# Optimization experiments

Measured on AMD Instinct MI355X. Metric: run time of the kernel, lower is better.

## Reference

```python
import jax, jax.numpy as jnp
import numpy as np

B, S, Dm, H, W, G = 2, 4096, 768, 12, 256, 16
HD = Dm // H
NEG = -10000.0


def _band_qk(q, k, w):
    # q,k: [B,S,H,D] -> banded scores [B,S,H,2w+1]; slot j = key position i-w+j
    Bq, Sq, Hq, Dq = q.shape
    nb = Sq // w
    qb = q.reshape(Bq, nb, w, Hq, Dq)
    kp = jnp.pad(k, ((0, 0), (w, w), (0, 0), (0, 0)))
    idx = (jnp.arange(nb) * w)[:, None] + jnp.arange(3 * w)[None, :]
    kb = kp[:, idx]                                    # [B,nb,3w,H,D]
    s = jnp.einsum('btxhd,btyhd->bthxy', qb, kb)       # [B,nb,H,w,3w]
    r = jnp.arange(w)[:, None]
    c = r + jnp.arange(2 * w + 1)[None, :]
    band = s[..., r, c]                                # [B,nb,H,w,2w+1]
    return band.transpose(0, 1, 3, 2, 4).reshape(Bq, Sq, Hq, 2 * w + 1)


def _band_pv(p, v, w):
    # p: [B,S,H,2w+1], v: [B,S,H,D] -> [B,S,H,D]
    Bp, Sp, Hp, _ = p.shape
    Dv = v.shape[-1]
    nb = Sp // w
    vp = jnp.pad(v, ((0, 0), (w, w), (0, 0), (0, 0)))
    idx = (jnp.arange(nb) * w)[:, None] + jnp.arange(3 * w)[None, :]
    vb = vp[:, idx]                                    # [B,nb,3w,H,D]
    pb = p.reshape(Bp, nb, w, Hp, 2 * w + 1).transpose(0, 1, 3, 2, 4)
    r = jnp.arange(w)[:, None]
    c = r + jnp.arange(2 * w + 1)[None, :]
    pband = jnp.zeros((Bp, nb, Hp, w, 3 * w), p.dtype).at[..., r, c].set(pb)
    out = jnp.einsum('bthxy,btyhd->btxhd', pband, vb)  # [B,nb,w,H,D]
    return out.reshape(Bp, Sp, Hp, Dv)


def setup_inputs() -> dict:
    key = jax.random.key(0)
    ks = jax.random.split(key, 13)
    inp = {'hidden_states': jax.random.normal(ks[0], (B, S, Dm), dtype=jnp.float32)}
    names = ['Wq', 'bq', 'Wk', 'bk', 'Wv', 'bv', 'Wqg', 'bqg', 'Wkg', 'bkg', 'Wvg', 'bvg']
    for i, n in enumerate(names):
        sh = (Dm, Dm) if n.startswith('W') else (Dm,)
        inp[n] = 0.02 * jax.random.normal(ks[i + 1], sh, dtype=jnp.float32)
    inp['n_global'] = G
    return inp


def reference(hidden_states, Wq, bq, Wk, bk, Wv, bv, Wqg, bqg, Wkg, bkg, Wvg, bvg, n_global):
    Bh, Sh, D = hidden_states.shape
    hd = D // H
    w, g = W, n_global
    scale = 1.0 / jnp.sqrt(jnp.float32(hd))
    q = ((hidden_states @ Wq + bq) * scale).reshape(Bh, Sh, H, hd)
    k = (hidden_states @ Wk + bk).reshape(Bh, Sh, H, hd)
    v = (hidden_states @ Wv + bv).reshape(Bh, Sh, H, hd)
    # banded local attention scores (mask_invalid_locations -> -inf outside seq)
    band = _band_qk(q, k, w)                           # [B,S,H,2w+1]
    i = jnp.arange(Sh)[:, None]
    j = jnp.arange(2 * w + 1)[None, :]
    kpos = i - w + j                                   # key position per window slot
    valid = (kpos >= 0) & (kpos < Sh)
    band = jnp.where(valid[None, :, None, :], band, -jnp.inf)
    # remove global keys from windowed attention (-10000 float mask)
    band = band + jnp.where(valid & (kpos < g), NEG, 0.0)[None, :, None, :]
    # global columns: every query attends to global keys (local k projection)
    sel = jnp.einsum('bihd,bghd->bihg', q, k[:, :g])
    logits = jnp.concatenate([sel, band], axis=-1)     # [B,S,H,g+2w+1]
    probs = jax.nn.softmax(logits.astype(jnp.float32), axis=-1)
    attn = jnp.einsum('bihg,bghd->bihd', probs[..., :g], v[:, :g])
    attn = attn + _band_pv(probs[..., g:], v, w)       # [B,S,H,hd]
    # global token rows: full attention with global projections
    qg = ((hidden_states[:, :g] @ Wqg + bqg) * scale).reshape(Bh, g, H, hd)
    kg = (hidden_states @ Wkg + bkg).reshape(Bh, Sh, H, hd)
    vg = (hidden_states @ Wvg + bvg).reshape(Bh, Sh, H, hd)
    gl = jnp.einsum('bghd,bshd->bhgs', qg, kg)
    gp = jax.nn.softmax(gl.astype(jnp.float32), axis=-1)
    out_g = jnp.einsum('bhgs,bshd->bghd', gp, vg)      # [B,g,H,hd]
    attn = attn.at[:, :g].set(out_g)
    return attn.reshape(Bh, Sh, D)
```

## Files before the change

kernel.cpp:

```cpp
#include <hip/hip_runtime.h>

constexpr int Bc = 2, Sc = 4096, Dmc = 768, Hc = 12, HDc = 64, Wc = 256, Gc = 16;
constexpr int NCHG = 64;
constexpr float LOG2E = 1.4426950408889634f;
constexpr float SCALE2q = 0.125f * LOG2E;
constexpr float NEG2c = -10000.0f * LOG2E;

typedef __attribute__((ext_vector_type(8))) short s16x8;
typedef __attribute__((ext_vector_type(4))) short s16x4;
typedef __attribute__((ext_vector_type(4))) float f32x4;
typedef __attribute__((ext_vector_type(2))) unsigned int u32x2;

#define DEVINL __device__ __forceinline__

DEVINL float b2f(short x) {
  unsigned int u = ((unsigned int)(unsigned short)x) << 16;
  return __builtin_bit_cast(float, u);
}
DEVINL short f2b(float f) {
  unsigned int u = __builtin_bit_cast(unsigned int, f);
  unsigned int r = (u + 0x7fffu + ((u >> 16) & 1u)) >> 16;
  return (short)r;
}
DEVINL void gload16(const short* g, const short* l) {
  __builtin_amdgcn_global_load_lds(
      (const __attribute__((address_space(1))) void*)g,
      (__attribute__((address_space(3))) void*)l, 16, 0, 0);
}
DEVINL float max3f(float a, float b, float c) { return fmaxf(fmaxf(a, b), c); }

__global__ __launch_bounds__(256) void conv_bf16(
    const float* __restrict__ src, short* __restrict__ dst)
{
  const size_t i = ((size_t)blockIdx.x * 256 + threadIdx.x) * 8;
  f32x4 a = *(const f32x4*)(src + i);
  f32x4 c = *(const f32x4*)(src + i + 4);
  s16x8 r;
#pragma unroll
  for (int u = 0; u < 4; ++u) { r[u] = f2b(a[u]); r[4 + u] = f2b(c[u]); }
  *(s16x8*)(dst + i) = r;
}

__global__ __launch_bounds__(256) void transpose_w(
    const float* __restrict__ W0, const float* __restrict__ W1, const float* __restrict__ W2,
    short* __restrict__ T0, short* __restrict__ T1, short* __restrict__ T2)
{
  const float* W = blockIdx.z == 0 ? W0 : (blockIdx.z == 1 ? W1 : W2);
  short* T = blockIdx.z == 0 ? T0 : (blockIdx.z == 1 ? T1 : T2);
  __shared__ short t[32][33];
  const int k0 = blockIdx.x * 32, n0 = blockIdx.y * 32;
  const int a = threadIdx.x >> 3, cg = (threadIdx.x & 7) * 4;
  f32x4 v = *(const f32x4*)&W[(size_t)(k0 + a) * Dmc + n0 + cg];
#pragma unroll
  for (int u = 0; u < 4; ++u) t[a][cg + u] = f2b(v[u]);
  __syncthreads();
  s16x4 s;
#pragma unroll
  for (int u = 0; u < 4; ++u) s[u] = t[cg + u][a];
  *(s16x4*)&T[(size_t)(n0 + a) * Dmc + k0 + cg] = s;
}

__global__ __launch_bounds__(256) void gemm_fused(
    const short* __restrict__ X, const short* __restrict__ Wt,
    const float* __restrict__ b0, const float* __restrict__ b1, const float* __restrict__ b2,
    short* __restrict__ Y0, float scale0)
{
  __shared__ short lds[16384];
  char* ldsb = (char*)lds;
  const int tid = threadIdx.x, lane = tid & 63, wid = tid >> 6;
  const int gy = gridDim.y;

  const int rawd = blockIdx.x + 64 * blockIdx.y;
  const int wgid = (rawd & 7) * (gy * 8) + (rawd >> 3);
  const int mi0 = wgid / gy, ny = wgid - mi0 * gy;
  const int m0 = mi0 * 128;
  const int nch = ny / 6, ncol = (ny % 6) * 128;
  const int n0g = ny * 128;

  short* Y = Y0 + (size_t)nch * 6291456;
  const float* bias = nch == 0 ? b0 : (nch == 1 ? b1 : b2);
  const float scale = nch == 0 ? scale0 : 1.0f;

  const int lr = lane & 15, lq = lane >> 4;
  const int wm = (wid & 1) * 64, wn = (wid >> 1) * 64;

  const int l8 = lane >> 3, l7 = lane & 7;
  const int colsh = ((l7 * 16) ^ (l8 << 4)) >> 1;
  const short* Aptr[4];
  const short* Bptr[4];
#pragma unroll
  for (int i = 0; i < 4; ++i) {
    Aptr[i] = X  + (size_t)(m0  + wid * 32 + i * 8 + l8) * Dmc + colsh;
    Bptr[i] = Wt + (size_t)(n0g + wid * 32 + i * 8 + l8) * Dmc + colsh;
  }

  int arb[4][2], brb[4][2];
#pragma unroll
  for (int mi = 0; mi < 4; ++mi)
#pragma unroll
    for (int ks = 0; ks < 2; ++ks) {
      int row = wm + mi * 16 + lr;
      arb[mi][ks] = row * 128 + ((lq * 16 + ks * 64) ^ ((row & 7) << 4));
    }
#pragma unroll
  for (int ni = 0; ni < 4; ++ni)
#pragma unroll
    for (int ks = 0; ks < 2; ++ks) {
      int row = wn + ni * 16 + lr;
      brb[ni][ks] = 16384 + row * 128 + ((lq * 16 + ks * 64) ^ ((row & 7) << 4));
    }

  f32x4 acc[4][4] = {};

  for (int kt = 0; kt < 12; ++kt) {
    const int ko = kt * 64;
    if (kt) __syncthreads();
#pragma unroll
    for (int i = 0; i < 4; ++i) {
      gload16(Aptr[i] + ko, &lds[wid * 2048 + i * 512]);
      gload16(Bptr[i] + ko, &lds[8192 + wid * 2048 + i * 512]);
    }
    asm volatile("s_waitcnt vmcnt(0)" ::: "memory");
    __syncthreads();
#pragma unroll
    for (int ks = 0; ks < 2; ++ks) {
      s16x8 af[4], bf[4];
#pragma unroll
      for (int mi = 0; mi < 4; ++mi) af[mi] = *(const s16x8*)(ldsb + arb[mi][ks]);
#pragma unroll
      for (int ni = 0; ni < 4; ++ni) bf[ni] = *(const s16x8*)(ldsb + brb[ni][ks]);
#pragma unroll
      for (int mi = 0; mi < 4; ++mi)
#pragma unroll
        for (int ni = 0; ni < 4; ++ni)
          acc[mi][ni] = __builtin_amdgcn_mfma_f32_16x16x32_bf16(af[mi], bf[ni], acc[mi][ni], 0, 0, 0);
    }
  }

#pragma unroll
  for (int mi = 0; mi < 4; ++mi)
#pragma unroll
    for (int ni = 0; ni < 4; ++ni) {
      int col = ncol + wn + ni * 16 + lr;
      float bv_ = bias[col];
#pragma unroll
      for (int r = 0; r < 4; ++r) {
        int row = m0 + wm + mi * 16 + lq * 4 + r;
        Y[(size_t)row * Dmc + col] = f2b((acc[mi][ni][r] + bv_) * scale);
      }
    }
}

__global__ __launch_bounds__(256) void qg_proj(
    const float* __restrict__ hs, const float* __restrict__ Wqg,
    const float* __restrict__ bqg, short* __restrict__ qg)
{
  const int row = blockIdx.x;
  const int b = row / Gc, i = row % Gc;
  const int tid = threadIdx.x;
  const int n = blockIdx.y * 128 + (tid & 127);
  const int half = tid >> 7;
  __shared__ float x[Dmc];
  __shared__ float part[128];
  for (int c = tid; c < Dmc; c += 256)
    x[c] = b2f(f2b(hs[((size_t)(b * Sc + i)) * Dmc + c]));
  __syncthreads();
  float acc = 0.f;
#pragma unroll 4
  for (int c = half * 384; c < half * 384 + 384; ++c)
    acc = fmaf(x[c], b2f(f2b(Wqg[(size_t)c * Dmc + n])), acc);
  if (half) part[tid & 127] = acc;
  __syncthreads();
  if (!half)
    qg[(size_t)row * Dmc + n] = f2b((acc + part[tid] + bqg[n]) * SCALE2q);
}

__global__ __launch_bounds__(256) void local_attn_mfma(
    const short* __restrict__ q, const short* __restrict__ k,
    const short* __restrict__ v, float* __restrict__ out)
{
  const int raw = blockIdx.x + 64 * (blockIdx.y + 12 * blockIdx.z);
  const int swz = (raw & 7) * 192 + (raw >> 3);
  const int q0 = (swz & 63) * 64;
  const int h = (swz >> 6) % 12, b = swz / 768;
  const int tid = threadIdx.x, lane = tid & 63, wid = tid >> 6;

  __shared__ short Ks[4096];
  __shared__ short Vt[4096];
  __shared__ short Ps[4][1024];
  char* KsB = (char*)Ks;
  char* VtB = (char*)Vt;

  const int ql = lane & 15;
  const int lg = lane >> 4;
  const int qr = wid * 16 + ql;

  s16x8 qf[2];
  {
    const short* qp = q + ((size_t)(b * Sc + q0 + qr)) * Dmc + h * HDc + lg * 8;
    qf[0] = *(const s16x8*)qp;
    qf[1] = *(const s16x8*)(qp + 32);
  }

  f32x4 oacc[4] = {};
  float m_run = -INFINITY, l_run = 0.f;

  const int krow = tid >> 3, kcol16 = (tid & 7) * 16;
  const int vp = tid & 31, vo = tid >> 5;
  const size_t hoff = (size_t)h * HDc;
  const size_t brow = (size_t)b * Sc;

  const bool interior = (q0 >= 256) && (q0 <= Sc - 384);

  auto keyof = [&](int c) {
    int key = (c < Gc) ? c : q0 - 272 + c;
    return min(max(key, 0), Sc - 1);
  };

  const short *kp0, *kp1, *vp0, *vp1;
  s16x8 kreg0, kreg1, vreg0, vreg1;
  auto loadRegs = [&](int ch) {
    if (!interior || ch <= 1) {
      kp0 = k + (brow + keyof(ch * 64 + krow))       * Dmc + hoff + (kcol16 >> 1);
      kp1 = k + (brow + keyof(ch * 64 + 32 + krow))  * Dmc + hoff + (kcol16 >> 1);
      vp0 = v + (brow + keyof(ch * 64 + 2 * vp))      * Dmc + hoff + vo * 8;
      vp1 = v + (brow + keyof(ch * 64 + 2 * vp + 1))  * Dmc + hoff + vo * 8;
    } else {
      kp0 += 64 * Dmc; kp1 += 64 * Dmc; vp0 += 64 * Dmc; vp1 += 64 * Dmc;
    }
    kreg0 = *(const s16x8*)kp0;
    kreg1 = *(const s16x8*)kp1;
    vreg0 = *(const s16x8*)vp0;
    vreg1 = *(const s16x8*)vp1;
  };

  loadRegs(0);

  for (int ch = 0; ch < 10; ++ch) {
    __syncthreads();
    *(s16x8*)(KsB + krow * 128        + (kcol16 ^ ((krow & 7) << 4))) = kreg0;
    *(s16x8*)(KsB + (krow + 32) * 128 + (kcol16 ^ ((krow & 7) << 4))) = kreg1;
#pragma unroll
    for (int j = 0; j < 8; ++j) {
      int d = vo * 8 + j;
      unsigned int wrd = (unsigned int)(unsigned short)vreg0[j] |
                         ((unsigned int)(unsigned short)vreg1[j] << 16);
      *(unsigned int*)(VtB + d * 128 + ((4 * vp) ^ (j << 4))) = wrd;
    }
    if (ch < 9) loadRegs(ch + 1);
    __syncthreads();

    if (ch == 9 && wid != 3) continue;

    f32x4 sac[4] = {};
    __builtin_amdgcn_s_setprio(1);
#pragma unroll
    for (int kt = 0; kt < 4; ++kt) {
      int row = kt * 16 + ql;
#pragma unroll
      for (int sl = 0; sl < 2; ++sl) {
        s16x8 af = *(const s16x8*)(KsB + row * 128 + ((lg * 16 + sl * 64) ^ ((row & 7) << 4)));
        sac[kt] = __builtin_amdgcn_mfma_f32_16x16x32_bf16(af, qf[sl], sac[kt], 0, 0, 0);
      }
    }
    __builtin_amdgcn_s_setprio(0);

    bool needMask = (ch < 2) | (ch > 7) | (q0 < 272) | (q0 > Sc - 384);
    if (needMask) {
#pragma unroll
      for (int kt = 0; kt < 4; ++kt)
#pragma unroll
        for (int r = 0; r < 4; ++r) {
          int c = ch * 64 + kt * 16 + lg * 4 + r;
          if (c >= Gc) {
            float sv = sac[kt][r];
            int jj = c - Gc - qr;
            int kp2 = q0 - 272 + c;
            bool ok = (jj >= 0) & (jj <= 2 * Wc) & (kp2 >= 0) & (kp2 < Sc);
            sac[kt][r] = ok ? (sv + ((kp2 < Gc) ? NEG2c : 0.f)) : -INFINITY;
          }
        }
    }

    float t0 = max3f(sac[0][0], sac[0][1], sac[0][2]);
    float t1 = max3f(sac[0][3], sac[1][0], sac[1][1]);
    float t2 = max3f(sac[1][2], sac[1][3], sac[2][0]);
    float t3 = max3f(sac[2][1], sac[2][2], sac[2][3]);
    float t4 = max3f(sac[3][0], sac[3][1], sac[3][2]);
    float cm = fmaxf(max3f(t0, t1, t2), max3f(t3, t4, sac[3][3]));
    cm = fmaxf(cm, __shfl_xor(cm, 16));
    cm = fmaxf(cm, __shfl_xor(cm, 32));

    if (__all(cm <= m_run + 11.5f)) {
      float cl0 = 0.f, cl1 = 0.f, cl2 = 0.f, cl3 = 0.f;
#pragma unroll
      for (int kt = 0; kt < 4; ++kt) {
        float p0 = __builtin_amdgcn_exp2f(sac[kt][0] - m_run);
        float p1 = __builtin_amdgcn_exp2f(sac[kt][1] - m_run);
        float p2 = __builtin_amdgcn_exp2f(sac[kt][2] - m_run);
        float p3 = __builtin_amdgcn_exp2f(sac[kt][3] - m_run);
        sac[kt][0] = p0; sac[kt][1] = p1; sac[kt][2] = p2; sac[kt][3] = p3;
        cl0 += p0; cl1 += p1; cl2 += p2; cl3 += p3;
      }
      float cl = (cl0 + cl1) + (cl2 + cl3);
      cl += __shfl_xor(cl, 16);
      cl += __shfl_xor(cl, 32);
      l_run += cl;
    } else {
      float m_new = fmaxf(m_run, cm);
      float scale = __builtin_amdgcn_exp2f(m_run - m_new);
      float cl0 = 0.f, cl1 = 0.f, cl2 = 0.f, cl3 = 0.f;
#pragma unroll
      for (int kt = 0; kt < 4; ++kt) {
        float p0 = __builtin_amdgcn_exp2f(sac[kt][0] - m_new);
        float p1 = __builtin_amdgcn_exp2f(sac[kt][1] - m_new);
        float p2 = __builtin_amdgcn_exp2f(sac[kt][2] - m_new);
        float p3 = __builtin_amdgcn_exp2f(sac[kt][3] - m_new);
        sac[kt][0] = p0; sac[kt][1] = p1; sac[kt][2] = p2; sac[kt][3] = p3;
        cl0 += p0; cl1 += p1; cl2 += p2; cl3 += p3;
      }
      float cl = (cl0 + cl1) + (cl2 + cl3);
      cl += __shfl_xor(cl, 16);
      cl += __shfl_xor(cl, 32);
      l_run = l_run * scale + cl;
      m_run = m_new;
#pragma unroll
      for (int rr = 0; rr < 4; ++rr) {
        float os = __shfl(scale, lg * 4 + rr);
#pragma unroll
        for (int dt = 0; dt < 4; ++dt) oacc[dt][rr] *= os;
      }
    }

    char* PsB = (char*)Ps[wid];
#pragma unroll
    for (int kt = 0; kt < 4; ++kt) {
      u32x2 pw;
      asm("v_cvt_pk_bf16_f32 %0, %1, %2" : "=v"(pw.x) : "v"(sac[kt][0]), "v"(sac[kt][1]));
      asm("v_cvt_pk_bf16_f32 %0, %1, %2" : "=v"(pw.y) : "v"(sac[kt][2]), "v"(sac[kt][3]));
      *(u32x2*)(PsB + ql * 128 + ((kt * 32 + lg * 8) ^ ((ql & 7) << 4))) = pw;
    }
    s16x8 pf[2];
#pragma unroll
    for (int ks = 0; ks < 2; ++ks)
      pf[ks] = *(const s16x8*)(PsB + ql * 128 + ((ks * 64 + lg * 16) ^ ((ql & 7) << 4)));
    __builtin_amdgcn_s_setprio(1);
#pragma unroll
    for (int dt = 0; dt < 4; ++dt) {
      int d = dt * 16 + ql;
#pragma unroll
      for (int ks = 0; ks < 2; ++ks) {
        s16x8 vf = *(const s16x8*)(VtB + d * 128 + ((ks * 64 + lg * 16) ^ ((d & 7) << 4)));
        oacc[dt] = __builtin_amdgcn_mfma_f32_16x16x32_bf16(pf[ks], vf, oacc[dt], 0, 0, 0);
      }
    }
    __builtin_amdgcn_s_setprio(0);
  }

  float inv = 1.f / l_run;
#pragma unroll
  for (int rr = 0; rr < 4; ++rr) {
    float oi = __shfl(inv, lg * 4 + rr);
    int row = q0 + wid * 16 + lg * 4 + rr;
    float* op = out + ((size_t)(b * Sc + row)) * Dmc + h * HDc + ql;
#pragma unroll
    for (int dt = 0; dt < 4; ++dt)
      op[dt * 16] = oacc[dt][rr] * oi;
  }
}

__global__ __launch_bounds__(64) void global_attn_part_mfma(
    const short* __restrict__ qg, const short* __restrict__ kg,
    const short* __restrict__ vg, float* __restrict__ pml, float* __restrict__ po)
{
  const int ch = blockIdx.x, h = blockIdx.y, b = blockIdx.z;
  const int lane = threadIdx.x;

  __shared__ short Ks[4096];
  __shared__ short Vt[4096];
  __shared__ short Ps[1024];
  char* KsB = (char*)Ks;
  char* VtB = (char*)Vt;

  const int ql = lane & 15;
  const int lg = lane >> 4;

  s16x8 qf[2];
  {
    const short* qp = qg + ((size_t)(b * Gc + ql)) * Dmc + h * HDc + lg * 8;
    qf[0] = *(const s16x8*)qp;
    qf[1] = *(const s16x8*)(qp + 32);
  }

  const size_t hoff = (size_t)h * HDc;
  const size_t brow = (size_t)b * Sc;
  const int key0 = ch * 64;

  const int krow = lane >> 3, kcol16 = (lane & 7) * 16;
#pragma unroll
  for (int rr = 0; rr < 8; ++rr) {
    int row = krow + rr * 8;
    s16x8 kv = *(const s16x8*)(kg + (brow + key0 + row) * Dmc + hoff + (kcol16 >> 1));
    *(s16x8*)(KsB + row * 128 + (kcol16 ^ ((row & 7) << 4))) = kv;
  }
  const int vp = lane & 31, vo0 = lane >> 5;
#pragma unroll
  for (int oo = 0; oo < 4; ++oo) {
    int vo = vo0 + oo * 2;
    s16x8 v0 = *(const s16x8*)(vg + (brow + key0 + 2 * vp)     * Dmc + hoff + vo * 8);
    s16x8 v1 = *(const s16x8*)(vg + (brow + key0 + 2 * vp + 1) * Dmc + hoff + vo * 8);
#pragma unroll
    for (int j = 0; j < 8; ++j) {
      int d = vo * 8 + j;
      unsigned int wrd = (unsigned int)(unsigned short)v0[j] |
                         ((unsigned int)(unsigned short)v1[j] << 16);
      *(unsigned int*)(VtB + d * 128 + ((4 * vp) ^ (j << 4))) = wrd;
    }
  }

  f32x4 sac[4] = {};
#pragma unroll
  for (int kt = 0; kt < 4; ++kt) {
    int row = kt * 16 + ql;
#pragma unroll
    for (int sl = 0; sl < 2; ++sl) {
      s16x8 af = *(const s16x8*)(KsB + row * 128 + ((lg * 16 + sl * 64) ^ ((row & 7) << 4)));
      sac[kt] = __builtin_amdgcn_mfma_f32_16x16x32_bf16(af, qf[sl], sac[kt], 0, 0, 0);
    }
  }

  float t0 = max3f(sac[0][0], sac[0][1], sac[0][2]);
  float t1 = max3f(sac[0][3], sac[1][0], sac[1][1]);
  float t2 = max3f(sac[1][2], sac[1][3], sac[2][0]);
  float t3 = max3f(sac[2][1], sac[2][2], sac[2][3]);
  float t4 = max3f(sac[3][0], sac[3][1], sac[3][2]);
  float m = fmaxf(max3f(t0, t1, t2), max3f(t3, t4, sac[3][3]));
  m = fmaxf(m, __shfl_xor(m, 16));
  m = fmaxf(m, __shfl_xor(m, 32));

  float cl = 0.f;
#pragma unroll
  for (int kt = 0; kt < 4; ++kt)
#pragma unroll
    for (int r = 0; r < 4; ++r) {
      float p = __builtin_amdgcn_exp2f(sac[kt][r] - m);
      sac[kt][r] = p;
      cl += p;
    }
  cl += __shfl_xor(cl, 16);
  cl += __shfl_xor(cl, 32);

#pragma unroll
  for (int kt = 0; kt < 4; ++kt) {
    u32x2 pw;
    asm("v_cvt_pk_bf16_f32 %0, %1, %2" : "=v"(pw.x) : "v"(sac[kt][0]), "v"(sac[kt][1]));
    asm("v_cvt_pk_bf16_f32 %0, %1, %2" : "=v"(pw.y) : "v"(sac[kt][2]), "v"(sac[kt][3]));
    *(u32x2*)((char*)Ps + ql * 128 + ((kt * 32 + lg * 8) ^ ((ql & 7) << 4))) = pw;
  }
  s16x8 pf[2];
#pragma unroll
  for (int ks = 0; ks < 2; ++ks)
    pf[ks] = *(const s16x8*)((char*)Ps + ql * 128 + ((ks * 64 + lg * 16) ^ ((ql & 7) << 4)));

  f32x4 oacc[4] = {};
#pragma unroll
  for (int dt = 0; dt < 4; ++dt) {
    int d = dt * 16 + ql;
#pragma unroll
    for (int ks = 0; ks < 2; ++ks) {
      s16x8 vf = *(const s16x8*)(VtB + d * 128 + ((ks * 64 + lg * 16) ^ ((d & 7) << 4)));
      oacc[dt] = __builtin_amdgcn_mfma_f32_16x16x32_bf16(pf[ks], vf, oacc[dt], 0, 0, 0);
    }
  }

  const size_t slot = ((size_t)(b * Hc + h) * NCHG + ch);
  float* pob = po + slot * 1024;
#pragma unroll
  for (int rr = 0; rr < 4; ++rr) {
    int qrow = lg * 4 + rr;
#pragma unroll
    for (int dt = 0; dt < 4; ++dt)
      pob[qrow * 64 + dt * 16 + ql] = oacc[dt][rr];
  }
  if (lg == 0) {
    pml[(slot * 16 + ql) * 2]     = m;
    pml[(slot * 16 + ql) * 2 + 1] = cl;
  }
}

__global__ __launch_bounds__(64) void global_attn_comb(
    const float* __restrict__ pml, const float* __restrict__ po,
    float* __restrict__ out)
{
  const int i = blockIdx.x, h = blockIdx.y, b = blockIdx.z;
  const int d = threadIdx.x;
  const size_t base = (size_t)(b * Hc + h) * NCHG;

  float m = -INFINITY;
#pragma unroll 8
  for (int ch = 0; ch < NCHG; ++ch) m = fmaxf(m, pml[((base + ch) * 16 + i) * 2]);
  float l = 0.f, o = 0.f;
#pragma unroll 8
  for (int ch = 0; ch < NCHG; ++ch) {
    float wgt = __builtin_amdgcn_exp2f(pml[((base + ch) * 16 + i) * 2] - m);
    l = fmaf(pml[((base + ch) * 16 + i) * 2 + 1], wgt, l);
    o = fmaf(po[(base + ch) * 1024 + i * 64 + d], wgt, o);
  }
  out[((size_t)(b * Sc + i)) * Dmc + h * HDc + d] = o / l;
}

extern "C" void kernel_launch(void* const* d_in, const int* in_sizes, int n_in,
                              void* d_out, int out_size, void* d_ws, size_t ws_size,
                              hipStream_t stream) {
  const float* hs  = (const float*)d_in[0];
  const float* Wq  = (const float*)d_in[1];
  const float* bq  = (const float*)d_in[2];
  const float* Wk  = (const float*)d_in[3];
  const float* bk  = (const float*)d_in[4];
  const float* Wv  = (const float*)d_in[5];
  const float* bv  = (const float*)d_in[6];
  const float* Wqg = (const float*)d_in[7];
  const float* bqg = (const float*)d_in[8];
  const float* Wkg = (const float*)d_in[9];
  const float* bkg = (const float*)d_in[10];
  const float* Wvg = (const float*)d_in[11];
  const float* bvg = (const float*)d_in[12];
  float* out = (float*)d_out;

  char* ws = (char*)d_ws;
  const size_t bufB = (size_t)Bc * Sc * Dmc * sizeof(short);
  short* hsb = (short*)(ws);
  short* s1  = (short*)(ws + bufB);
  short* s2  = (short*)(ws + 2 * bufB);
  short* s3  = (short*)(ws + 3 * bufB);

  short* wtA = (short*)d_out;
  short* wtB = wtA + (size_t)Dmc * Dmc;
  short* wtC = wtB + (size_t)Dmc * Dmc;
  short* qgb = (short*)(ws + 3 * bufB);
  float* pml = (float*)(ws + 3 * bufB + 65536);
  float* po  = (float*)(ws + 3 * bufB + (1u << 20));
  short* wtD = (short*)(ws + 3 * bufB + (8u << 20));
  short* wtE = wtD + (size_t)Dmc * Dmc;

  dim3 bb(256);
  conv_bf16<<<dim3(3072), bb, 0, stream>>>(hs, hsb);
  transpose_w<<<dim3(24, 24, 3), bb, 0, stream>>>(Wq, Wk, Wv, wtA, wtB, wtC);

  gemm_fused<<<dim3(64, 18), bb, 0, stream>>>(hsb, wtA, bq, bk, bv, s1, SCALE2q);

  local_attn_mfma<<<dim3(64, Hc, Bc), bb, 0, stream>>>(s1, s2, s3, out);

  transpose_w<<<dim3(24, 24, 2), bb, 0, stream>>>(Wkg, Wvg, Wvg, wtD, wtE, wtE);
  gemm_fused<<<dim3(64, 12), bb, 0, stream>>>(hsb, wtD, bkg, bvg, bvg, s1, 1.0f);

  qg_proj<<<dim3(Bc * Gc, Dmc / 128), bb, 0, stream>>>(hs, Wqg, bqg, qgb);
  global_attn_part_mfma<<<dim3(NCHG, Hc, Bc), dim3(64), 0, stream>>>(qgb, s1, s2, pml, po);
  global_attn_comb<<<dim3(Gc, Hc, Bc), dim3(64), 0, stream>>>(pml, po, out);
}
```

Measured before the change: 176.9 us.

## Merge all five projection GEMMs and weight transposes into single launches

Combines the Q/K/V and global K/V weight transposes into one five-slice launch and runs all five projection GEMMs as one 64x30 grid. The global K/V results are staged in the output buffer, and the global partial attention runs before local attention, which then overwrites that buffer. The aim is to cut kernel launches and fill the GPU better with one larger GEMM grid. This depends on the workspace being big enough, with the old sequence kept as a fallback, and on global_attn_part finishing before local attention writes to the output.

```diff
diff --git a/kernel.cpp b/kernel.cpp
--- a/kernel.cpp
+++ b/kernel.cpp
@@ -5,6 +5,7 @@
 constexpr float LOG2E = 1.4426950408889634f;
 constexpr float SCALE2q = 0.125f * LOG2E;
 constexpr float NEG2c = -10000.0f * LOG2E;
+constexpr size_t BUFE = 6291456;
 
 typedef __attribute__((ext_vector_type(8))) short s16x8;
 typedef __attribute__((ext_vector_type(4))) short s16x4;
@@ -41,12 +42,14 @@
   *(s16x8*)(dst + i) = r;
 }
 
-__global__ __launch_bounds__(256) void transpose_w(
-    const float* __restrict__ W0, const float* __restrict__ W1, const float* __restrict__ W2,
-    short* __restrict__ T0, short* __restrict__ T1, short* __restrict__ T2)
-{
-  const float* W = blockIdx.z == 0 ? W0 : (blockIdx.z == 1 ? W1 : W2);
-  short* T = blockIdx.z == 0 ? T0 : (blockIdx.z == 1 ? T1 : T2);
+__global__ __launch_bounds__(256) void transpose_w5(
+    const float* __restrict__ W0, const float* __restrict__ W1,
+    const float* __restrict__ W2, const float* __restrict__ W3,
+    const float* __restrict__ W4, short* __restrict__ Tbase)
+{
+  const int z = blockIdx.z;
+  const float* W = z == 0 ? W0 : (z == 1 ? W1 : (z == 2 ? W2 : (z == 3 ? W3 : W4)));
+  short* T = Tbase + (size_t)z * Dmc * Dmc;
   __shared__ short t[32][33];
   const int k0 = blockIdx.x * 32, n0 = blockIdx.y * 32;
   const int a = threadIdx.x >> 3, cg = (threadIdx.x & 7) * 4;
@@ -60,10 +63,12 @@
   *(s16x4*)&T[(size_t)(n0 + a) * Dmc + k0 + cg] = s;
 }
 
-__global__ __launch_bounds__(256) void gemm_fused(
+__global__ __launch_bounds__(256) void gemm_all(
     const short* __restrict__ X, const short* __restrict__ Wt,
-    const float* __restrict__ b0, const float* __restrict__ b1, const float* __restrict__ b2,
-    short* __restrict__ Y0, float scale0)
+    const float* __restrict__ b0, const float* __restrict__ b1,
+    const float* __restrict__ b2, const float* __restrict__ b3,
+    const float* __restrict__ b4,
+    short* __restrict__ Yws, short* __restrict__ Yout, float scale0)
 {
   __shared__ short lds[16384];
   char* ldsb = (char*)lds;
@@ -77,8 +82,8 @@
   const int nch = ny / 6, ncol = (ny % 6) * 128;
   const int n0g = ny * 128;
 
-  short* Y = Y0 + (size_t)nch * 6291456;
-  const float* bias = nch == 0 ? b0 : (nch == 1 ? b1 : b2);
+  short* Y = (nch < 3) ? (Yws + (size_t)nch * BUFE) : (Yout + (size_t)(nch - 3) * BUFE);
+  const float* bias = nch == 0 ? b0 : (nch == 1 ? b1 : (nch == 2 ? b2 : (nch == 3 ? b3 : b4)));
   const float scale = nch == 0 ? scale0 : 1.0f;
 
   const int lr = lane & 15, lq = lane >> 4;
@@ -529,32 +534,47 @@
 
   char* ws = (char*)d_ws;
   const size_t bufB = (size_t)Bc * Sc * Dmc * sizeof(short);
+  const size_t wt5B = 5ull * Dmc * Dmc * sizeof(short);
   short* hsb = (short*)(ws);
-  short* s1  = (short*)(ws + bufB);
-  short* s2  = (short*)(ws + 2 * bufB);
-  short* s3  = (short*)(ws + 3 * bufB);
-
-  short* wtA = (short*)d_out;
-  short* wtB = wtA + (size_t)Dmc * Dmc;
-  short* wtC = wtB + (size_t)Dmc * Dmc;
-  short* qgb = (short*)(ws + 3 * bufB);
-  float* pml = (float*)(ws + 3 * bufB + 65536);
-  float* po  = (float*)(ws + 3 * bufB + (1u << 20));
-  short* wtD = (short*)(ws + 3 * bufB + (8u << 20));
-  short* wtE = wtD + (size_t)Dmc * Dmc;
+  short* qb  = (short*)(ws + bufB);
 
   dim3 bb(256);
-  conv_bf16<<<dim3(3072), bb, 0, stream>>>(hs, hsb);
-  transpose_w<<<dim3(24, 24, 3), bb, 0, stream>>>(Wq, Wk, Wv, wtA, wtB, wtC);
-
-  gemm_fused<<<dim3(64, 18), bb, 0, stream>>>(hsb, wtA, bq, bk, bv, s1, SCALE2q);
-
-  local_attn_mfma<<<dim3(64, Hc, Bc), bb, 0, stream>>>(s1, s2, s3, out);
-
-  transpose_w<<<dim3(24, 24, 2), bb, 0, stream>>>(Wkg, Wvg, Wvg, wtD, wtE, wtE);
-  gemm_fused<<<dim3(64, 12), bb, 0, stream>>>(hsb, wtD, bkg, bvg, bvg, s1, 1.0f);
-
-  qg_proj<<<dim3(Bc * Gc, Dmc / 128), bb, 0, stream>>>(hs, Wqg, bqg, qgb);
-  global_attn_part_mfma<<<dim3(NCHG, Hc, Bc), dim3(64), 0, stream>>>(qgb, s1, s2, pml, po);
-  global_attn_comb<<<dim3(Gc, Hc, Bc), dim3(64), 0, stream>>>(pml, po, out);
-}
+
+  if (ws_size >= 4 * bufB + wt5B) {
+    short* wt5 = (short*)(ws + 4 * bufB);
+    short* qgb = (short*)(ws);
+    float* pml = (float*)(ws + 262144);
+    float* po  = (float*)(ws + (1u << 20));
+    short* kgb = (short*)d_out;
+    short* vgb = kgb + BUFE;
+
+    conv_bf16<<<dim3(3072), bb, 0, stream>>>(hs, hsb);
+    transpose_w5<<<dim3(24, 24, 5), bb, 0, stream>>>(Wq, Wk, Wv, Wkg, Wvg, wt5);
+    gemm_all<<<dim3(64, 30), bb, 0, stream>>>(hsb, wt5, bq, bk, bv, bkg, bvg,
+                                              qb, kgb, SCALE2q);
+    qg_proj<<<dim3(Bc * Gc, Dmc / 128), bb, 0, stream>>>(hs, Wqg, bqg, qgb);
+    global_attn_part_mfma<<<dim3(NCHG, Hc, Bc), dim3(64), 0, stream>>>(qgb, kgb, vgb, pml, po);
+    local_attn_mfma<<<dim3(64, Hc, Bc), bb, 0, stream>>>(qb, qb + BUFE, qb + 2 * BUFE, out);
+    global_attn_comb<<<dim3(Gc, Hc, Bc), dim3(64), 0, stream>>>(pml, po, out);
+  } else {
+    short* wtA = (short*)d_out;
+    short* qgb = (short*)(ws + 3 * bufB);
+    float* pml = (float*)(ws + 3 * bufB + 262144);
+    float* po  = (float*)(ws + 3 * bufB + (1u << 20));
+    short* wtD = (short*)(ws + 3 * bufB + (8u << 20));
+    short* kgb = qb;
+    short* vgb = qb + BUFE;
+
+    conv_bf16<<<dim3(3072), bb, 0, stream>>>(hs, hsb);
+    transpose_w5<<<dim3(24, 24, 3), bb, 0, stream>>>(Wq, Wk, Wv, Wv, Wv, wtA);
+    gemm_all<<<dim3(64, 18), bb, 0, stream>>>(hsb, wtA, bq, bk, bv, bv, bv,
+                                              qb, qb, SCALE2q);
+    local_attn_mfma<<<dim3(64, Hc, Bc), bb, 0, stream>>>(qb, qb + BUFE, qb + 2 * BUFE, out);
+    transpose_w5<<<dim3(24, 24, 2), bb, 0, stream>>>(Wkg, Wvg, Wvg, Wvg, Wvg, wtD);
+    gemm_all<<<dim3(64, 12), bb, 0, stream>>>(hsb, wtD, bkg, bvg, bvg, bvg, bvg,
+                                              kgb, kgb, 1.0f);
+    qg_proj<<<dim3(Bc * Gc, Dmc / 128), bb, 0, stream>>>(hs, Wqg, bqg, qgb);
+    global_attn_part_mfma<<<dim3(NCHG, Hc, Bc), dim3(64), 0, stream>>>(qgb, kgb, vgb, pml, po);
+    global_attn_comb<<<dim3(Gc, Hc, Bc), dim3(64), 0, stream>>>(pml, po, out);
+  }
+}
```

Result: no change. 174.7 us (-1.2%).
